# Optimization experiments

Measured on AMD Instinct MI355X. Metric: run time of the kernel, lower is better.

## Reference

```python
import jax, jax.numpy as jnp
import numpy as np


def _sobel_kernels(dtype):
    # kornia sobel order=1, normalized: divide by sum(|k|)=8
    gx = jnp.array([[-1., 0., 1.], [-2., 0., 2.], [-1., 0., 1.]], dtype=dtype) / 8.0
    gy = gx.T
    return jnp.stack([gx, gy])[:, None]  # (2, 1, 3, 3) OIHW


def _spatial_gradient(x):
    # x: (b, c, h, w) -> gx, gy each (b, c, h, w)
    b, c, h, w = x.shape
    xp = jnp.pad(x.reshape(b * c, 1, h, w), ((0, 0), (0, 0), (1, 1), (1, 1)), mode='edge')
    k = _sobel_kernels(x.dtype)
    out = jax.lax.conv_general_dilated(
        xp, k, window_strides=(1, 1), padding='VALID',
        dimension_numbers=('NCHW', 'OIHW', 'NCHW'))  # (b*c, 2, h, w)
    out = out.reshape(b, c, 2, h, w)
    return out[:, :, 0], out[:, :, 1]


def setup_inputs() -> dict:
    key = jax.random.key(0)
    x = jax.random.normal(key, (16, 3, 512, 512), dtype=jnp.float32)
    return {"x": x}


def reference(x):
    b, c, h, w = x.shape
    gx, gy = _spatial_gradient(x)  # (b, c, h, w) each
    if c == 3:
        mag_c = jnp.sqrt(gx * gx + gy * gy + 1e-9)  # per-channel magnitude
        # first-occurrence argmax over channels matches torch .max(dim) tie-break
        idx = jnp.argmax(mag_c, axis=1)  # (b, h, w)
        gxs = jnp.take_along_axis(gx, idx[:, None], axis=1)[:, 0]  # (b, h, w)
        gys = jnp.take_along_axis(gy, idx[:, None], axis=1)[:, 0]
    else:
        gxs, gys = gx, gy
    magnitude = jnp.sqrt(gxs * gxs + gys * gys + 1e-9)
    # clipped_div(gx, gy, 10.0)
    y_tr = jnp.where(gys == 0.0, jnp.asarray(1e-9, gys.dtype), gys)
    angle = jnp.clip(gxs / y_tr, -10.0, 10.0)
    return magnitude, angle
```

## Files before the change

### kernel.cpp

```cpp
#include <hip/hip_runtime.h>


constexpr int Hc = 512;
constexpr int Wc = 512;
constexpr int Cc = 3;
constexpr int PW = 8;
constexpr int TPR = Wc / PW;

__global__ __launch_bounds__(256, 4) void sobel_mag_angle_kernel(
    const float* __restrict__ x, float* __restrict__ out, int B) {
    int tid = blockIdx.x * 256 + threadIdx.x;
    int lane = tid & (TPR - 1);
    int h = (tid / TPR) & (Hc - 1);
    int b = tid / (TPR * Hc);
    int w0 = lane * PW;

    const float* xb = x + (size_t)b * Cc * Hc * Wc;
    int hm = h > 0 ? h - 1 : 0;
    int hp = h < Hc - 1 ? h + 1 : h;
    int wl = w0 > 0 ? w0 - 1 : 0;
    int wr = w0 + PW < Wc ? w0 + PW : Wc - 1;

    float bm[PW], bgx[PW], bgy[PW];

#pragma unroll
    for (int c = 0; c < Cc; ++c) {
        const float* base = xb + c * (Hc * Wc);
        const float* pm = base + hm * Wc;
        const float* pc = base + h * Wc;
        const float* pp = base + hp * Wc;
        float4 a0 = *(const float4*)(pm + w0), a1 = *(const float4*)(pm + w0 + 4);
        float4 b0 = *(const float4*)(pc + w0), b1 = *(const float4*)(pc + w0 + 4);
        float4 c0 = *(const float4*)(pp + w0), c1 = *(const float4*)(pp + w0 + 4);
        float lm = pm[wl], rm = pm[wr];
        float lc = pc[wl], rc = pc[wr];
        float lp = pp[wl], rp = pp[wr];
        float r0[10] = {lm, a0.x, a0.y, a0.z, a0.w, a1.x, a1.y, a1.z, a1.w, rm};
        float r1[10] = {lc, b0.x, b0.y, b0.z, b0.w, b1.x, b1.y, b1.z, b1.w, rc};
        float r2[10] = {lp, c0.x, c0.y, c0.z, c0.w, c1.x, c1.y, c1.z, c1.w, rp};
#pragma unroll
        for (int i = 0; i < PW; ++i) {
            float t0 = r0[i + 2] - r0[i];
            float t1 = r1[i + 2] - r1[i];
            float t2 = r2[i + 2] - r2[i];
            float gx = 0.125f * (t0 + t2) + 0.25f * t1;
            float u0 = r2[i]     - r0[i];
            float u1 = r2[i + 1] - r0[i + 1];
            float u2 = r2[i + 2] - r0[i + 2];
            float gy = 0.125f * (u0 + u2) + 0.25f * u1;
            float m = __builtin_amdgcn_sqrtf(gx * gx + gy * gy + 1e-9f);
            if (c == 0) {
                bm[i] = m; bgx[i] = gx; bgy[i] = gy;
            } else {
                bool gt = m > bm[i];
                bm[i] = gt ? m : bm[i];
                bgx[i] = gt ? gx : bgx[i];
                bgy[i] = gt ? gy : bgy[i];
            }
        }
    }

    float mo[PW], ao[PW];
#pragma unroll
    for (int i = 0; i < PW; ++i) {
        mo[i] = bm[i];
        float yt = (bgy[i] == 0.0f) ? 1e-9f : bgy[i];
        float a = bgx[i] * __builtin_amdgcn_rcpf(yt);
        ao[i] = fminf(fmaxf(a, -10.0f), 10.0f);
    }

    size_t obase = ((size_t)b * Hc + h) * Wc + w0;
    size_t npix = (size_t)B * Hc * Wc;
    *(float4*)(out + obase)            = make_float4(mo[0], mo[1], mo[2], mo[3]);
    *(float4*)(out + obase + 4)        = make_float4(mo[4], mo[5], mo[6], mo[7]);
    *(float4*)(out + npix + obase)     = make_float4(ao[0], ao[1], ao[2], ao[3]);
    *(float4*)(out + npix + obase + 4) = make_float4(ao[4], ao[5], ao[6], ao[7]);
}

extern "C" void kernel_launch(void* const* d_in, const int* in_sizes, int n_in,
                              void* d_out, int out_size, void* d_ws, size_t ws_size,
                              hipStream_t stream) {
    const float* x = (const float*)d_in[0];
    float* out = (float*)d_out;
    int B = in_sizes[0] / (Cc * Hc * Wc);
    int total_threads = B * Hc * TPR;
    int blocks = total_threads / 256;
    sobel_mag_angle_kernel<<<blocks, 256, 0, stream>>>(x, out, B);
}
```

Baseline: 106.4 us.

## Compute two output rows per thread and fetch halo pixels via wavefront shuffles

Each thread now produces two consecutive output rows, loading four input rows per channel instead of three per output row, so vertical neighbour rows are reused in registers. The scalar left and right halo loads are replaced by cross-lane shuffles within the 64-wide wavefront, which works because each wavefront covers exactly one full image row. This cuts global load instructions and redundant traffic at the cost of more registers per thread and half as many threads.

```diff
diff --git a/kernel.cpp b/kernel.cpp
--- a/kernel.cpp
+++ b/kernel.cpp
@@ -5,76 +5,87 @@
 constexpr int Wc = 512;
 constexpr int Cc = 3;
 constexpr int PW = 8;
+constexpr int RT = 2;
 constexpr int TPR = Wc / PW;
 
 __global__ __launch_bounds__(256, 4) void sobel_mag_angle_kernel(
     const float* __restrict__ x, float* __restrict__ out, int B) {
     int tid = blockIdx.x * 256 + threadIdx.x;
-    int lane = tid & (TPR - 1);
-    int h = (tid / TPR) & (Hc - 1);
-    int b = tid / (TPR * Hc);
-    int w0 = lane * PW;
+    int lane = tid & 63;
+    int hh = (tid >> 6) & (Hc / RT - 1);
+    int b = tid >> 14;
+    int w0 = lane << 3;
+    int h0 = hh * RT;
 
     const float* xb = x + (size_t)b * Cc * Hc * Wc;
-    int hm = h > 0 ? h - 1 : 0;
-    int hp = h < Hc - 1 ? h + 1 : h;
-    int wl = w0 > 0 ? w0 - 1 : 0;
-    int wr = w0 + PW < Wc ? w0 + PW : Wc - 1;
+    int rm = h0 > 0 ? h0 - 1 : 0;
+    int rp = h0 + RT < Hc ? h0 + RT : Hc - 1;
 
-    float bm[PW], bgx[PW], bgy[PW];
+    bool l0 = (lane == 0), l63 = (lane == 63);
+
+    float bm[RT][PW], bgx[RT][PW], bgy[RT][PW];
 
 #pragma unroll
     for (int c = 0; c < Cc; ++c) {
         const float* base = xb + c * (Hc * Wc);
-        const float* pm = base + hm * Wc;
-        const float* pc = base + h * Wc;
-        const float* pp = base + hp * Wc;
-        float4 a0 = *(const float4*)(pm + w0), a1 = *(const float4*)(pm + w0 + 4);
-        float4 b0 = *(const float4*)(pc + w0), b1 = *(const float4*)(pc + w0 + 4);
-        float4 c0 = *(const float4*)(pp + w0), c1 = *(const float4*)(pp + w0 + 4);
-        float lm = pm[wl], rm = pm[wr];
-        float lc = pc[wl], rc = pc[wr];
-        float lp = pp[wl], rp = pp[wr];
-        float r0[10] = {lm, a0.x, a0.y, a0.z, a0.w, a1.x, a1.y, a1.z, a1.w, rm};
-        float r1[10] = {lc, b0.x, b0.y, b0.z, b0.w, b1.x, b1.y, b1.z, b1.w, rc};
-        float r2[10] = {lp, c0.x, c0.y, c0.z, c0.w, c1.x, c1.y, c1.z, c1.w, rp};
+        const float* pr[4] = { base + rm * Wc, base + h0 * Wc,
+                               base + (h0 + 1) * Wc, base + rp * Wc };
+        float row[4][10];
 #pragma unroll
-        for (int i = 0; i < PW; ++i) {
-            float t0 = r0[i + 2] - r0[i];
-            float t1 = r1[i + 2] - r1[i];
-            float t2 = r2[i + 2] - r2[i];
-            float gx = 0.125f * (t0 + t2) + 0.25f * t1;
-            float u0 = r2[i]     - r0[i];
-            float u1 = r2[i + 1] - r0[i + 1];
-            float u2 = r2[i + 2] - r0[i + 2];
-            float gy = 0.125f * (u0 + u2) + 0.25f * u1;
-            float m = __builtin_amdgcn_sqrtf(gx * gx + gy * gy + 1e-9f);
-            if (c == 0) {
-                bm[i] = m; bgx[i] = gx; bgy[i] = gy;
-            } else {
-                bool gt = m > bm[i];
-                bm[i] = gt ? m : bm[i];
-                bgx[i] = gt ? gx : bgx[i];
-                bgy[i] = gt ? gy : bgy[i];
+        for (int r = 0; r < 4; ++r) {
+            float4 v0 = *(const float4*)(pr[r] + w0);
+            float4 v1 = *(const float4*)(pr[r] + w0 + 4);
+            float lh = __shfl_up(v1.w, 1);
+            lh = l0 ? v0.x : lh;
+            float rh = __shfl_down(v0.x, 1);
+            rh = l63 ? v1.w : rh;
+            row[r][0] = lh;
+            row[r][1] = v0.x; row[r][2] = v0.y; row[r][3] = v0.z; row[r][4] = v0.w;
+            row[r][5] = v1.x; row[r][6] = v1.y; row[r][7] = v1.z; row[r][8] = v1.w;
+            row[r][9] = rh;
+        }
+#pragma unroll
+        for (int rr = 0; rr < RT; ++rr) {
+#pragma unroll
+            for (int i = 0; i < PW; ++i) {
+                float t0 = row[rr][i + 2]     - row[rr][i];
+                float t1 = row[rr + 1][i + 2] - row[rr + 1][i];
+                float t2 = row[rr + 2][i + 2] - row[rr + 2][i];
+                float gx = 0.125f * (t0 + t2) + 0.25f * t1;
+                float u0 = row[rr + 2][i]     - row[rr][i];
+                float u1 = row[rr + 2][i + 1] - row[rr][i + 1];
+                float u2 = row[rr + 2][i + 2] - row[rr][i + 2];
+                float gy = 0.125f * (u0 + u2) + 0.25f * u1;
+                float m = __builtin_amdgcn_sqrtf(gx * gx + gy * gy + 1e-9f);
+                if (c == 0) {
+                    bm[rr][i] = m; bgx[rr][i] = gx; bgy[rr][i] = gy;
+                } else {
+                    bool gt = m > bm[rr][i];
+                    bm[rr][i]  = gt ? m  : bm[rr][i];
+                    bgx[rr][i] = gt ? gx : bgx[rr][i];
+                    bgy[rr][i] = gt ? gy : bgy[rr][i];
+                }
             }
         }
     }
 
-    float mo[PW], ao[PW];
+    size_t npix = (size_t)B * Hc * Wc;
 #pragma unroll
-    for (int i = 0; i < PW; ++i) {
-        mo[i] = bm[i];
-        float yt = (bgy[i] == 0.0f) ? 1e-9f : bgy[i];
-        float a = bgx[i] * __builtin_amdgcn_rcpf(yt);
-        ao[i] = fminf(fmaxf(a, -10.0f), 10.0f);
+    for (int rr = 0; rr < RT; ++rr) {
+        float mo[PW], ao[PW];
+#pragma unroll
+        for (int i = 0; i < PW; ++i) {
+            mo[i] = bm[rr][i];
+            float yt = (bgy[rr][i] == 0.0f) ? 1e-9f : bgy[rr][i];
+            float a = bgx[rr][i] * __builtin_amdgcn_rcpf(yt);
+            ao[i] = fminf(fmaxf(a, -10.0f), 10.0f);
+        }
+        size_t obase = ((size_t)b * Hc + (h0 + rr)) * Wc + w0;
+        *(float4*)(out + obase)            = make_float4(mo[0], mo[1], mo[2], mo[3]);
+        *(float4*)(out + obase + 4)        = make_float4(mo[4], mo[5], mo[6], mo[7]);
+        *(float4*)(out + npix + obase)     = make_float4(ao[0], ao[1], ao[2], ao[3]);
+        *(float4*)(out + npix + obase + 4) = make_float4(ao[4], ao[5], ao[6], ao[7]);
     }
-
-    size_t obase = ((size_t)b * Hc + h) * Wc + w0;
-    size_t npix = (size_t)B * Hc * Wc;
-    *(float4*)(out + obase)            = make_float4(mo[0], mo[1], mo[2], mo[3]);
-    *(float4*)(out + obase + 4)        = make_float4(mo[4], mo[5], mo[6], mo[7]);
-    *(float4*)(out + npix + obase)     = make_float4(ao[0], ao[1], ao[2], ao[3]);
-    *(float4*)(out + npix + obase + 4) = make_float4(ao[4], ao[5], ao[6], ao[7]);
 }
 
 extern "C" void kernel_launch(void* const* d_in, const int* in_sizes, int n_in,
@@ -83,7 +94,7 @@
     const float* x = (const float*)d_in[0];
     float* out = (float*)d_out;
     int B = in_sizes[0] / (Cc * Hc * Wc);
-    int total_threads = B * Hc * TPR;
+    int total_threads = B * (Hc / RT) * TPR;
     int blocks = total_threads / 256;
     sobel_mag_angle_kernel<<<blocks, 256, 0, stream>>>(x, out, B);
 }
```

Result: faster. 101.8 us (-4.4%).
